# Kernel tuning notes

Measured on AMD Instinct MI355X. Metric: run time of the kernel, lower is better.

The kernel has to match this reference:

```python
import jax, jax.numpy as jnp
import numpy as np

A, B, O, ACT, H, NH = 16, 8192, 128, 16, 128, 4
D = H // NH  # attend_dim
IN = O + ACT
NEG = -1e9


def setup_inputs() -> dict:
    key = jax.random.key(0)
    ks = jax.random.split(key, 16)
    s = lambda k, shape, fan: jax.random.normal(k, shape, jnp.float32) / np.sqrt(fan)
    return {
        "obs": jax.random.normal(ks[0], (A, B, O), jnp.float32),
        "actions": jax.random.uniform(ks[1], (A, B, ACT), jnp.float32),
        # per-agent sa-encoder (enc_fc1)
        "W_sa": s(ks[2], (A, IN, H), IN), "b_sa": jnp.zeros((A, H), jnp.float32),
        # per-agent state encoder (s_enc_fc1)
        "W_s": s(ks[3], (A, O, H), O), "b_s": jnp.zeros((A, H), jnp.float32),
        # shared per-head extractors
        "Wk": s(ks[4], (NH, H, D), H),
        "Wsel": s(ks[5], (NH, H, D), H),
        "Wv": s(ks[6], (NH, H, D), H), "bv": jnp.zeros((NH, D), jnp.float32),
        # per-agent critic MLP
        "Wc1": s(ks[7], (A, 2 * H, H), 2 * H), "bc1": jnp.zeros((A, H), jnp.float32),
        "Wc2": s(ks[8], (A, H, ACT), H), "bc2": jnp.zeros((A, ACT), jnp.float32),
    }


def _bn(x):
    # BatchNorm1d(affine=False) in training mode: normalize over batch axis, biased var
    m = x.mean(axis=1, keepdims=True)
    v = x.var(axis=1, keepdims=True)
    return (x - m) / jnp.sqrt(v + 1e-5)


def reference(obs, actions, W_sa, b_sa, W_s, b_s, Wk, Wsel, Wv, bv, Wc1, bc1, Wc2, bc2):
    lrelu = jax.nn.leaky_relu  # slope 0.01, matches torch default
    inp = jnp.concatenate([obs, actions], axis=-1)            # [A,B,IN]
    sa = lrelu(jnp.einsum('abi,aih->abh', _bn(inp), W_sa) + b_sa[:, None, :])  # [A,B,H]
    se = lrelu(jnp.einsum('abo,aoh->abh', _bn(obs), W_s) + b_s[:, None, :])    # [A,B,H]
    keys = jnp.einsum('abh,nhd->nabd', sa, Wk)                # [NH,A,B,D]
    vals = lrelu(jnp.einsum('abh,nhd->nabd', sa, Wv) + bv[:, None, None, :])
    sel = jnp.einsum('abh,nhd->nabd', se, Wsel)
    logits = jnp.einsum('nibd,njbd->nibj', sel, keys) / np.sqrt(D)  # [NH,A,B,A]
    self_mask = jnp.eye(A, dtype=bool)[None, :, None, :]      # mask j == i
    w = jax.nn.softmax(jnp.where(self_mask, NEG, logits), axis=-1)
    other = jnp.einsum('nibj,njbd->nibd', w, vals)            # [NH,A,B,D]
    other = jnp.transpose(other, (1, 2, 0, 3)).reshape(A, B, NH * D)  # head-order concat
    cin = jnp.concatenate([se, other], axis=-1)               # [A,B,2H]
    h = lrelu(jnp.einsum('abk,akh->abh', cin, Wc1) + bc1[:, None, :])
    all_q = jnp.einsum('abh,aho->abo', h, Wc2) + bc2[:, None, :]      # [A,B,ACT]
    idx = jnp.argmax(actions, axis=-1)[..., None]             # int_acs, [A,B,1]
    q = jnp.take_along_axis(all_q, idx, axis=-1)              # [A,B,1]
    return q
```

## Files before the change

### kernel.cpp

```cpp
#include <hip/hip_runtime.h>
#include <hip/hip_bf16.h>

#define A_N 16
#define B_N 8192
#define O_N 128
#define ACT_N 16
#define H_N 128
#define NH_N 4
#define D_N 32
#define IN_N 144
#define NEGV -1e9f

typedef __attribute__((ext_vector_type(8))) short short8;
typedef __attribute__((ext_vector_type(4))) float floatx4;

static __device__ inline unsigned short f2bf(float f) {
    union { float f; unsigned u; } x{f};
    unsigned u = x.u + 0x7FFFu + ((x.u >> 16) & 1u);
    return (unsigned short)(u >> 16);
}
static __device__ inline unsigned pack_bf2(float a, float b) {
    union { float f; unsigned u; } xa{a}, xb{b};
    unsigned ua = xa.u + 0x7FFFu + ((xa.u >> 16) & 1u);
    unsigned ub = xb.u + 0x7FFFu + ((xb.u >> 16) & 1u);
    return (ua >> 16) | (ub & 0xFFFF0000u);
}
static __device__ inline float bf2f(unsigned short h) {
    union { unsigned u; float f; } x;
    x.u = ((unsigned)h) << 16;
    return x.f;
}
static __device__ inline float bflo(unsigned u) {
    union { unsigned u; float f; } x; x.u = u << 16; return x.f;
}
static __device__ inline float bfhi(unsigned u) {
    union { unsigned u; float f; } x; x.u = u & 0xFFFF0000u; return x.f;
}
static __device__ inline short8 ld_frag(const unsigned* p) {
    union { unsigned u[4]; short8 v; } x;
    uint2 lo = *(const uint2*)p;
    uint2 hi = *(const uint2*)(p + 2);
    x.u[0] = lo.x; x.u[1] = lo.y; x.u[2] = hi.x; x.u[3] = hi.y;
    return x.v;
}

__global__ __launch_bounds__(256) void k_zero(float* p, int n) {
    int i = blockIdx.x * 256 + threadIdx.x;
    if (i < n) p[i] = 0.f;
}

__global__ __launch_bounds__(256) void k_stats(const float* __restrict__ obs,
                                               const float* __restrict__ act,
                                               float* __restrict__ gsum,
                                               float* __restrict__ gsq) {
    __shared__ float ssum[IN_N];
    __shared__ float ssq[IN_N];
    int a = blockIdx.x >> 5;
    int r0 = (blockIdx.x & 31) * 256;
    int t = threadIdx.x;
    if (t < IN_N) { ssum[t] = 0.f; ssq[t] = 0.f; }
    __syncthreads();
    if (t < 128) {
        const float* p = obs + ((size_t)a * B_N + r0) * O_N + t;
        float s = 0.f, q = 0.f;
#pragma unroll 4
        for (int r = 0; r < 256; ++r) {
            float v = p[(size_t)r * O_N];
            s += v; q += v * v;
        }
        ssum[t] = s; ssq[t] = q;
    } else {
        int tt = t - 128;
        int f = tt & 15, rg = tt >> 4;
        const float* p = act + ((size_t)a * B_N + r0 + rg) * ACT_N + f;
        float s = 0.f, q = 0.f;
#pragma unroll 4
        for (int i = 0; i < 32; ++i) {
            float v = p[(size_t)i * 8 * ACT_N];
            s += v; q += v * v;
        }
        atomicAdd(&ssum[O_N + f], s);
        atomicAdd(&ssq[O_N + f], q);
    }
    __syncthreads();
    if (t < IN_N) {
        atomicAdd(&gsum[a * IN_N + t], ssum[t]);
        atomicAdd(&gsq[a * IN_N + t], ssq[t]);
    }
}

__global__ __launch_bounds__(256) void k_finalize(float* gsum, float* gsq) {
    int i = blockIdx.x * 256 + threadIdx.x;
    if (i < A_N * IN_N) {
        const float invB = 1.f / (float)B_N;
        float m = gsum[i] * invB;
        float v = fmaxf(gsq[i] * invB - m * m, 0.f);
        gsum[i] = m;
        gsq[i] = rsqrtf(v + 1e-5f);
    }
}

#define L1E 393216
#define P1E 409600
#define P2E 417792
#define CRE 679936
#define C2E 712704
__global__ __launch_bounds__(256) void k_wprep(
    const float* __restrict__ W_sa, const float* __restrict__ W_s,
    const float* __restrict__ Wk, const float* __restrict__ Wsel,
    const float* __restrict__ Wv, const float* __restrict__ Wc1,
    const float* __restrict__ Wc2, const float* __restrict__ rstd,
    unsigned* __restrict__ wt_l1, unsigned* __restrict__ wt_p1,
    unsigned* __restrict__ wt_p2, unsigned* __restrict__ wt_cr,
    float* __restrict__ wt_c2) {
    int idx = blockIdx.x * 256 + threadIdx.x;
    if (idx < L1E) {
        int a = idx / 24576, rem = idx % 24576;
        int n = rem & 255, kp = rem >> 8;
        int k0 = 2 * kp, k1 = k0 + 1;
        float v0 = 0.f, v1 = 0.f;
        if (n < 128) {
            if (k0 < IN_N) v0 = W_sa[((size_t)a * IN_N + k0) * H_N + n] * rstd[a * IN_N + k0];
            if (k1 < IN_N) v1 = W_sa[((size_t)a * IN_N + k1) * H_N + n] * rstd[a * IN_N + k1];
        } else {
            int m = n - 128;
            if (k0 < O_N) v0 = W_s[((size_t)a * O_N + k0) * H_N + m] * rstd[a * IN_N + k0];
            if (k1 < O_N) v1 = W_s[((size_t)a * O_N + k1) * H_N + m] * rstd[a * IN_N + k1];
        }
        wt_l1[(size_t)a * 24576 + n * 96 + kp] = pack_bf2(v0, v1);
    } else if (idx < P1E) {
        int i2 = idx - L1E;
        int n = i2 & 255, kp = i2 >> 8;
        int k0 = 2 * kp;
        float v0, v1;
        if (n < 128) {
            const float* w = Wk + ((size_t)(n >> 5) * H_N) * D_N + (n & 31);
            v0 = w[(size_t)k0 * D_N]; v1 = w[(size_t)(k0 + 1) * D_N];
        } else {
            int m = n - 128;
            const float* w = Wv + ((size_t)(m >> 5) * H_N) * D_N + (m & 31);
            v0 = w[(size_t)k0 * D_N]; v1 = w[(size_t)(k0 + 1) * D_N];
        }
        wt_p1[n * 64 + kp] = pack_bf2(v0, v1);
    } else if (idx < P2E) {
        int i3 = idx - P1E;
        int n = i3 & 127, kp = i3 >> 7;
        int k0 = 2 * kp;
        const float* w = Wsel + ((size_t)(n >> 5) * H_N) * D_N + (n & 31);
        wt_p2[n * 64 + kp] = pack_bf2(w[(size_t)k0 * D_N], w[(size_t)(k0 + 1) * D_N]);
    } else if (idx < CRE) {
        int i4 = idx - P2E;
        int a = i4 >> 14, r = i4 & 16383;
        int n = r & 127, kp = r >> 7;
        int k0 = 2 * kp;
        const float* w = Wc1 + (size_t)a * 256 * H_N + n;
        wt_cr[(size_t)a * 16384 + n * 128 + kp] =
            pack_bf2(w[(size_t)k0 * H_N], w[(size_t)(k0 + 1) * H_N]);
    } else if (idx < C2E) {
        int i5 = idx - CRE;
        int a = i5 >> 11, rem = i5 & 2047;
        int oo = rem >> 7, h = rem & 127;
        wt_c2[i5] = Wc2[((size_t)a * H_N + h) * ACT_N + oo];
    }
}

__global__ __launch_bounds__(256) void k_bfold(
    const float* __restrict__ mean, const float* __restrict__ rstd,
    const float* __restrict__ W_sa, const float* __restrict__ W_s,
    const float* __restrict__ b_sa, const float* __restrict__ b_s,
    float* __restrict__ fb) {
    int a = blockIdx.x, c = threadIdx.x;
    float s = 0.f;
    if (c < 128) {
        for (int k = 0; k < IN_N; ++k)
            s += mean[a * IN_N + k] * rstd[a * IN_N + k] *
                 W_sa[((size_t)a * IN_N + k) * H_N + c];
        fb[a * 128 + c] = b_sa[a * H_N + c] - s;
    } else {
        int m = c - 128;
        for (int k = 0; k < O_N; ++k)
            s += mean[a * IN_N + k] * rstd[a * IN_N + k] *
                 W_s[((size_t)a * O_N + k) * H_N + m];
        fb[2048 + a * 128 + m] = b_s[a * H_N + m] - s;
    }
}

__global__ __launch_bounds__(512, 2) void k_l1(
    const float* __restrict__ obs, const float* __restrict__ act,
    const unsigned* __restrict__ wt_l1, const float* __restrict__ fb,
    unsigned short* __restrict__ sa_us, unsigned short* __restrict__ se_us,
    int b0g, int Bc) {
    __shared__ unsigned smem[(128 + 256) * 34];
    unsigned* Xs = smem;
    unsigned* Ws = smem + 128 * 34;

    int a = blockIdx.y;
    int b0 = blockIdx.x * 128;
    int t = threadIdx.x;
    int wid = t >> 6, lane = t & 63, lm = lane & 15, lq = lane >> 4;
    int wrow = (wid & 1) * 64;
    int wcol = (wid >> 1) * 64;

    floatx4 acc[4][4];
#pragma unroll
    for (int mt = 0; mt < 4; ++mt)
#pragma unroll
        for (int nt = 0; nt < 4; ++nt)
#pragma unroll
            for (int e = 0; e < 4; ++e) acc[mt][nt][e] = 0.f;

    const unsigned* WtA = wt_l1 + (size_t)a * 24576;

    for (int c = 0; c < 3; ++c) {
        int kk = c * 64;
        __syncthreads();
        for (int idx = t; idx < 128 * 16; idx += 512) {
            int r = idx >> 4, c4 = idx & 15;
            int k = kk + c4 * 4;
            size_t grow = (size_t)a * B_N + b0g + b0 + r;
            float4 v;
            if (k < O_N) v = *(const float4*)&obs[grow * O_N + k];
            else if (k < IN_N) v = *(const float4*)&act[grow * ACT_N + (k - O_N)];
            else v = make_float4(0.f, 0.f, 0.f, 0.f);
            uint2* dst = (uint2*)&Xs[r * 34 + c4 * 2];
            *dst = make_uint2(pack_bf2(v.x, v.y), pack_bf2(v.z, v.w));
        }
        for (int idx = t; idx < 256 * 8; idx += 512) {
            int n = idx >> 3, c4 = idx & 7;
            uint4 w = *(const uint4*)&WtA[(size_t)n * 96 + (kk >> 1) + c4 * 4];
            uint2* dst = (uint2*)&Ws[n * 34 + c4 * 4];
            dst[0] = make_uint2(w.x, w.y);
            dst[1] = make_uint2(w.z, w.w);
        }
        __syncthreads();
#pragma unroll
        for (int s = 0; s < 2; ++s) {
            if (kk + s * 32 >= 160) break;
            short8 afr[4];
#pragma unroll
            for (int mt = 0; mt < 4; ++mt)
                afr[mt] = ld_frag(&Xs[(wrow + mt * 16 + lm) * 34 + s * 16 + lq * 4]);
#pragma unroll
            for (int nt = 0; nt < 4; ++nt) {
                short8 bfr = ld_frag(&Ws[(wcol + nt * 16 + lm) * 34 + s * 16 + lq * 4]);
#pragma unroll
                for (int mt = 0; mt < 4; ++mt)
                    acc[mt][nt] = __builtin_amdgcn_mfma_f32_16x16x32_bf16(
                        afr[mt], bfr, acc[mt][nt], 0, 0, 0);
            }
        }
    }

    int zsel = (wcol >= 128);
    unsigned short* outp = zsel ? se_us : sa_us;
    const float* bias = fb + zsel * 2048 + a * 128;
    int cbase = wcol & 127;
#pragma unroll
    for (int mt = 0; mt < 4; ++mt)
#pragma unroll
        for (int nt = 0; nt < 4; ++nt)
#pragma unroll
            for (int r = 0; r < 4; ++r) {
                int row = wrow + mt * 16 + lq * 4 + r;
                int col = cbase + nt * 16 + lm;
                float v = acc[mt][nt][r] + bias[col];
                v = v > 0.f ? v : 0.01f * v;
                outp[((size_t)(b0 + row) * 16 + a) * 128 + col] = f2bf(v);
            }
}

__global__ __launch_bounds__(256, 3) void k_fused(
    const unsigned* __restrict__ sa_u, const unsigned* __restrict__ se_u,
    const unsigned* __restrict__ wt_p1, const unsigned* __restrict__ wt_p2,
    const float* __restrict__ bv, unsigned short* __restrict__ other_us,
    int Bc) {
    __shared__ unsigned Xs[64 * 66];
    __shared__ unsigned short keys_s[64 * 130];
    __shared__ unsigned short vals_s[64 * 136];
    unsigned short* sel_s = (unsigned short*)Xs;

    int bg0 = blockIdx.x * 4;
    int t = threadIdx.x;
    int wid = t >> 6, lane = t & 63, lm = lane & 15, lq = lane >> 4;
    int wcol = wid * 32;

    const unsigned* sa_base = sa_u + (size_t)(bg0 * 16) * 64;
    const unsigned* se_base = se_u + (size_t)(bg0 * 16) * 64;

    for (int idx = t; idx < 64 * 16; idx += 256) {
        int r = idx >> 4, c4 = idx & 15;
        uint4 v = *(const uint4*)&sa_base[(size_t)idx * 4];
        uint2* dst = (uint2*)&Xs[r * 66 + c4 * 4];
        dst[0] = make_uint2(v.x, v.y);
        dst[1] = make_uint2(v.z, v.w);
    }
    uint4 seR[4];
#pragma unroll
    for (int ii = 0; ii < 4; ++ii) {
        int idx = t + ii * 256;
        seR[ii] = *(const uint4*)&se_base[(size_t)idx * 4];
    }
    __syncthreads();

#pragma unroll
    for (int pass = 0; pass < 2; ++pass) {
        floatx4 acc[4][2];
#pragma unroll
        for (int mt = 0; mt < 4; ++mt)
#pragma unroll
            for (int nt = 0; nt < 2; ++nt)
#pragma unroll
                for (int e = 0; e < 4; ++e) acc[mt][nt][e] = 0.f;
        const unsigned* wbase = wt_p1 + (size_t)(pass * 128) * 64;
#pragma unroll
        for (int s = 0; s < 4; ++s) {
            short8 afr[4];
#pragma unroll
            for (int mt = 0; mt < 4; ++mt)
                afr[mt] = ld_frag(&Xs[(mt * 16 + lm) * 66 + s * 16 + lq * 4]);
#pragma unroll
            for (int nt = 0; nt < 2; ++nt) {
                int col = wcol + nt * 16 + lm;
                short8 bfr = ld_frag(wbase + (size_t)col * 64 + s * 16 + lq * 4);
#pragma unroll
                for (int mt = 0; mt < 4; ++mt)
                    acc[mt][nt] = __builtin_amdgcn_mfma_f32_16x16x32_bf16(
                        afr[mt], bfr, acc[mt][nt], 0, 0, 0);
            }
        }
#pragma unroll
        for (int mt = 0; mt < 4; ++mt)
#pragma unroll
            for (int nt = 0; nt < 2; ++nt)
#pragma unroll
                for (int r = 0; r < 4; ++r) {
                    int row = mt * 16 + lq * 4 + r;
                    int col = wcol + nt * 16 + lm;
                    float v = acc[mt][nt][r];
                    if (pass == 0) {
                        keys_s[row * 130 + col] = f2bf(v);
                    } else {
                        v += bv[col];
                        v = v > 0.f ? v : 0.01f * v;
                        vals_s[row * 136 + col] = f2bf(v);
                    }
                }
    }
    __syncthreads();

#pragma unroll
    for (int ii = 0; ii < 4; ++ii) {
        int idx = t + ii * 256;
        int r = idx >> 4, c4 = idx & 15;
        uint2* dst = (uint2*)&Xs[r * 66 + c4 * 4];
        dst[0] = make_uint2(seR[ii].x, seR[ii].y);
        dst[1] = make_uint2(seR[ii].z, seR[ii].w);
    }
    __syncthreads();

    {
        floatx4 acc[4][2];
#pragma unroll
        for (int mt = 0; mt < 4; ++mt)
#pragma unroll
            for (int nt = 0; nt < 2; ++nt)
#pragma unroll
                for (int e = 0; e < 4; ++e) acc[mt][nt][e] = 0.f;
#pragma unroll
        for (int s = 0; s < 4; ++s) {
            short8 afr[4];
#pragma unroll
            for (int mt = 0; mt < 4; ++mt)
                afr[mt] = ld_frag(&Xs[(mt * 16 + lm) * 66 + s * 16 + lq * 4]);
#pragma unroll
            for (int nt = 0; nt < 2; ++nt) {
                int col = wcol + nt * 16 + lm;
                short8 bfr = ld_frag(wt_p2 + (size_t)col * 64 + s * 16 + lq * 4);
#pragma unroll
                for (int mt = 0; mt < 4; ++mt)
                    acc[mt][nt] = __builtin_amdgcn_mfma_f32_16x16x32_bf16(
                        afr[mt], bfr, acc[mt][nt], 0, 0, 0);
            }
        }
        __syncthreads();
#pragma unroll
        for (int mt = 0; mt < 4; ++mt)
#pragma unroll
            for (int nt = 0; nt < 2; ++nt)
#pragma unroll
                for (int r = 0; r < 4; ++r) {
                    int row = mt * 16 + lq * 4 + r;
                    int col = wcol + nt * 16 + lm;
                    sel_s[row * 132 + col] = f2bf(acc[mt][nt][r]);
                }
    }
    __syncthreads();

    const unsigned* keysU = (const unsigned*)keys_s;
    floatx4 lgacc[4];
#pragma unroll
    for (int n = 0; n < 4; ++n) {
        short8 afr = ld_frag(&Xs[(wid * 16 + lm) * 66 + n * 16 + lq * 4]);
        short8 bfr = ld_frag(&keysU[(wid * 16 + lm) * 65 + n * 16 + lq * 4]);
        floatx4 z4 = {0.f, 0.f, 0.f, 0.f};
        lgacc[n] = __builtin_amdgcn_mfma_f32_16x16x32_bf16(afr, bfr, z4, 0, 0, 0);
    }
    __syncthreads();

    float* lgs = (float*)keys_s;
#pragma unroll
    for (int n = 0; n < 4; ++n)
#pragma unroll
        for (int r = 0; r < 4; ++r) {
            int i = lq * 4 + r;
            lgs[((wid * 4 + n) * 16 + i) * 16 + lm] =
                lgacc[n][r] * 0.17677669529663687f;
        }

    int bsub = wid, n = (t >> 4) & 3, i = t & 15;
    float lg[16];
    {
        const float4* lgp = (const float4*)&lgs[((bsub * 4 + n) * 16 + i) * 16];
#pragma unroll
        for (int c = 0; c < 4; ++c) {
            float4 v = lgp[c];
            lg[4 * c] = v.x; lg[4 * c + 1] = v.y;
            lg[4 * c + 2] = v.z; lg[4 * c + 3] = v.w;
        }
    }
    lg[i] = NEGV;
    float m = lg[0];
#pragma unroll
    for (int j = 1; j < 16; ++j) m = fmaxf(m, lg[j]);
    float sum = 0.f;
#pragma unroll
    for (int j = 0; j < 16; ++j) { lg[j] = __expf(lg[j] - m); sum += lg[j]; }
    float inv = 1.f / sum;
#pragma unroll
    for (int j = 0; j < 16; ++j) lg[j] *= inv;

    const unsigned* valsU = (const unsigned*)vals_s;
    float ov[32];
#pragma unroll
    for (int u = 0; u < 32; ++u) ov[u] = 0.f;
#pragma unroll
    for (int j = 0; j < 16; ++j) {
        const uint4* vrow = (const uint4*)&valsU[(bsub * 16 + j) * 68 + n * 16];
        float w = lg[j];
#pragma unroll
        for (int c = 0; c < 4; ++c) {
            uint4 x = vrow[c];
            ov[8 * c + 0] = fmaf(w, bflo(x.x), ov[8 * c + 0]);
            ov[8 * c + 1] = fmaf(w, bfhi(x.x), ov[8 * c + 1]);
            ov[8 * c + 2] = fmaf(w, bflo(x.y), ov[8 * c + 2]);
            ov[8 * c + 3] = fmaf(w, bfhi(x.y), ov[8 * c + 3]);
            ov[8 * c + 4] = fmaf(w, bflo(x.z), ov[8 * c + 4]);
            ov[8 * c + 5] = fmaf(w, bfhi(x.z), ov[8 * c + 5]);
            ov[8 * c + 6] = fmaf(w, bflo(x.w), ov[8 * c + 6]);
            ov[8 * c + 7] = fmaf(w, bfhi(x.w), ov[8 * c + 7]);
        }
    }
    {
        uint4* orow = (uint4*)&other_us[((size_t)(bg0 + bsub) * 16 + i) * 128 + n * 32];
#pragma unroll
        for (int h = 0; h < 2; ++h) {
            uint4 o;
            o.x = pack_bf2(ov[16 * h + 0], ov[16 * h + 1]);
            o.y = pack_bf2(ov[16 * h + 2], ov[16 * h + 3]);
            o.z = pack_bf2(ov[16 * h + 4], ov[16 * h + 5]);
            o.w = pack_bf2(ov[16 * h + 6], ov[16 * h + 7]);
            orow[2 * h] = o;
            o.x = pack_bf2(ov[16 * h + 8], ov[16 * h + 9]);
            o.y = pack_bf2(ov[16 * h + 10], ov[16 * h + 11]);
            o.z = pack_bf2(ov[16 * h + 12], ov[16 * h + 13]);
            o.w = pack_bf2(ov[16 * h + 14], ov[16 * h + 15]);
            orow[2 * h + 1] = o;
        }
    }
}

__global__ __launch_bounds__(256, 4) void k_critic(
    const unsigned* __restrict__ se_u, const unsigned* __restrict__ other_u,
    const unsigned* __restrict__ wt_cr,
    const float* __restrict__ bc1, const float* __restrict__ actions,
    const float* __restrict__ wt_c2, const float* __restrict__ bc2,
    float* __restrict__ qout, int b0g, int Bc) {
    __shared__ unsigned smem[(64 + 128) * 34];
    unsigned* Xs = smem;
    unsigned* Ws = smem + 64 * 34;

    int a = blockIdx.y;
    int b0 = blockIdx.x * 64;
    int t = threadIdx.x;
    int wid = t >> 6, lane = t & 63, lm = lane & 15, lq = lane >> 4;
    int wrow = (wid & 1) * 32;
    int wcol = (wid >> 1) * 64;

    floatx4 acc[2][4];
#pragma unroll
    for (int mt = 0; mt < 2; ++mt)
#pragma unroll
        for (int nt = 0; nt < 4; ++nt)
#pragma unroll
            for (int e = 0; e < 4; ++e) acc[mt][nt][e] = 0.f;

    const unsigned* WtA = wt_cr + (size_t)a * 16384;

    for (int c = 0; c < 4; ++c) {
        int kk = c * 64;
        __syncthreads();
        const unsigned* src = (c < 2) ? se_u : other_u;
        int off = (c & 1) * 32;
        for (int idx = t; idx < 64 * 8; idx += 256) {
            int r = idx >> 3, c4 = idx & 7;
            uint4 v = *(const uint4*)&src[((size_t)(b0 + r) * 16 + a) * 64 + off + c4 * 4];
            uint2* dst = (uint2*)&Xs[r * 34 + c4 * 4];
            dst[0] = make_uint2(v.x, v.y);
            dst[1] = make_uint2(v.z, v.w);
        }
        for (int idx = t; idx < 128 * 8; idx += 256) {
            int n = idx >> 3, c4 = idx & 7;
            uint4 w = *(const uint4*)&WtA[(size_t)n * 128 + (kk >> 1) + c4 * 4];
            uint2* dst = (uint2*)&Ws[n * 34 + c4 * 4];
            dst[0] = make_uint2(w.x, w.y);
            dst[1] = make_uint2(w.z, w.w);
        }
        __syncthreads();
#pragma unroll
        for (int s = 0; s < 2; ++s) {
            short8 afr[2];
#pragma unroll
            for (int mt = 0; mt < 2; ++mt)
                afr[mt] = ld_frag(&Xs[(wrow + mt * 16 + lm) * 34 + s * 16 + lq * 4]);
#pragma unroll
            for (int nt = 0; nt < 4; ++nt) {
                short8 bfr = ld_frag(&Ws[(wcol + nt * 16 + lm) * 34 + s * 16 + lq * 4]);
#pragma unroll
                for (int mt = 0; mt < 2; ++mt)
                    acc[mt][nt] = __builtin_amdgcn_mfma_f32_16x16x32_bf16(
                        afr[mt], bfr, acc[mt][nt], 0, 0, 0);
            }
        }
    }

    __syncthreads();
    unsigned short* hbuf = (unsigned short*)smem;
#pragma unroll
    for (int mt = 0; mt < 2; ++mt)
#pragma unroll
        for (int nt = 0; nt < 4; ++nt)
#pragma unroll
            for (int r = 0; r < 4; ++r) {
                int row = wrow + mt * 16 + lq * 4 + r;
                int col = wcol + nt * 16 + lm;
                float v = acc[mt][nt][r] + bc1[a * H_N + col];
                v = v > 0.f ? v : 0.01f * v;
                hbuf[row * 132 + col] = f2bf(v);
            }
    __syncthreads();
    if (t < 64) {
        size_t arow = (size_t)a * B_N + b0g + b0 + t;
        const float* ap = &actions[arow * ACT_N];
        float bestv = ap[0];
        int bi = 0;
        for (int o = 1; o < ACT_N; ++o) {
            float v = ap[o];
            if (v > bestv) { bestv = v; bi = o; }
        }
        float q = bc2[a * ACT_N + bi];
        const float4* w4p = (const float4*)&wt_c2[((size_t)a * ACT_N + bi) * H_N];
        const uint2* hp2 = (const uint2*)&hbuf[t * 132];
#pragma unroll
        for (int h4 = 0; h4 < 32; ++h4) {
            float4 w4 = w4p[h4];
            uint2 hh = hp2[h4];
            q = fmaf(bflo(hh.x), w4.x, q);
            q = fmaf(bfhi(hh.x), w4.y, q);
            q = fmaf(bflo(hh.y), w4.z, q);
            q = fmaf(bfhi(hh.y), w4.w, q);
        }
        qout[arow] = q;
    }
}

extern "C" void kernel_launch(void* const* d_in, const int* in_sizes, int n_in,
                              void* d_out, int out_size, void* d_ws, size_t ws_size,
                              hipStream_t stream) {
    const float* obs     = (const float*)d_in[0];
    const float* actions = (const float*)d_in[1];
    const float* W_sa    = (const float*)d_in[2];
    const float* b_sa    = (const float*)d_in[3];
    const float* W_s     = (const float*)d_in[4];
    const float* b_s     = (const float*)d_in[5];
    const float* Wk      = (const float*)d_in[6];
    const float* Wsel    = (const float*)d_in[7];
    const float* Wv      = (const float*)d_in[8];
    const float* bv      = (const float*)d_in[9];
    const float* Wc1     = (const float*)d_in[10];
    const float* bc1     = (const float*)d_in[11];
    const float* Wc2     = (const float*)d_in[12];
    const float* bc2     = (const float*)d_in[13];
    float* out = (float*)d_out;
    char* ws = (char*)d_ws;

    size_t o = 0;
    float* gsum = (float*)(ws + o); o += 2304 * 4;
    float* gsq  = (float*)(ws + o); o += 2304 * 4;
    unsigned* wt_l1 = (unsigned*)(ws + o); o += (size_t)393216 * 4;
    unsigned* wt_p1 = (unsigned*)(ws + o); o += (size_t)16384 * 4;
    unsigned* wt_p2 = (unsigned*)(ws + o); o += (size_t)8192 * 4;
    unsigned* wt_cr = (unsigned*)(ws + o); o += (size_t)262144 * 4;
    float* fb = (float*)(ws + o); o += (size_t)4096 * 4;
    float* wt_c2 = (float*)(ws + o); o += (size_t)32768 * 4;
    size_t fixed = o;

    int Bc = B_N;
    while (Bc > 128 && fixed + 12288ull * Bc > ws_size) Bc >>= 1;

    unsigned short* sa_us = (unsigned short*)(ws + o); o += (size_t)A_N * Bc * 128 * 2;
    unsigned short* se_us = (unsigned short*)(ws + o); o += (size_t)A_N * Bc * 128 * 2;
    unsigned short* ot_us = (unsigned short*)(ws + o); o += (size_t)A_N * Bc * 128 * 2;

    k_zero<<<dim3(18), 256, 0, stream>>>(gsum, 2 * A_N * IN_N);
    k_stats<<<dim3(A_N * 32), 256, 0, stream>>>(obs, actions, gsum, gsq);
    k_finalize<<<dim3(9), 256, 0, stream>>>(gsum, gsq);
    k_wprep<<<dim3(C2E / 256), 256, 0, stream>>>(W_sa, W_s, Wk, Wsel, Wv, Wc1, Wc2,
                                                 gsq, wt_l1, wt_p1, wt_p2, wt_cr, wt_c2);
    k_bfold<<<dim3(A_N), 256, 0, stream>>>(gsum, gsq, W_sa, W_s, b_sa, b_s, fb);

    for (int b0g = 0; b0g < B_N; b0g += Bc) {
        k_l1<<<dim3(Bc / 128, A_N), 512, 0, stream>>>(
            obs, actions, wt_l1, fb, sa_us, se_us, b0g, Bc);
        k_fused<<<dim3(Bc / 4), 256, 0, stream>>>(
            (const unsigned*)sa_us, (const unsigned*)se_us, wt_p1, wt_p2, bv,
            ot_us, Bc);
        k_critic<<<dim3(Bc / 64, A_N), 256, 0, stream>>>(
            (const unsigned*)se_us, (const unsigned*)ot_us, wt_cr, bc1,
            actions, wt_c2, bc2, out, b0g, Bc);
    }
}
```

Measured before the change: 317.7 us.

## Make fused attention kernel wave-private, dropping block-wide barriers and shared input staging

```diff
diff --git a/kernel.cpp b/kernel.cpp
--- a/kernel.cpp
+++ b/kernel.cpp
@@ -41,6 +41,11 @@
     uint2 lo = *(const uint2*)p;
     uint2 hi = *(const uint2*)(p + 2);
     x.u[0] = lo.x; x.u[1] = lo.y; x.u[2] = hi.x; x.u[3] = hi.y;
+    return x.v;
+}
+static __device__ inline short8 ld_frag4(const unsigned* p) {
+    union { uint4 q; short8 v; } x;
+    x.q = *(const uint4*)p;
     return x.v;
 }
 
@@ -274,153 +279,98 @@
     const unsigned* __restrict__ wt_p1, const unsigned* __restrict__ wt_p2,
     const float* __restrict__ bv, unsigned short* __restrict__ other_us,
     int Bc) {
-    __shared__ unsigned Xs[64 * 66];
-    __shared__ unsigned short keys_s[64 * 130];
-    __shared__ unsigned short vals_s[64 * 136];
-    unsigned short* sel_s = (unsigned short*)Xs;
-
-    int bg0 = blockIdx.x * 4;
+    __shared__ unsigned short lds[4][3][16][136];
+
     int t = threadIdx.x;
     int wid = t >> 6, lane = t & 63, lm = lane & 15, lq = lane >> 4;
-    int wcol = wid * 32;
-
-    const unsigned* sa_base = sa_u + (size_t)(bg0 * 16) * 64;
-    const unsigned* se_base = se_u + (size_t)(bg0 * 16) * 64;
-
-    for (int idx = t; idx < 64 * 16; idx += 256) {
-        int r = idx >> 4, c4 = idx & 15;
-        uint4 v = *(const uint4*)&sa_base[(size_t)idx * 4];
-        uint2* dst = (uint2*)&Xs[r * 66 + c4 * 4];
-        dst[0] = make_uint2(v.x, v.y);
-        dst[1] = make_uint2(v.z, v.w);
-    }
-    uint4 seR[4];
-#pragma unroll
-    for (int ii = 0; ii < 4; ++ii) {
-        int idx = t + ii * 256;
-        seR[ii] = *(const uint4*)&se_base[(size_t)idx * 4];
-    }
-    __syncthreads();
-
-#pragma unroll
-    for (int pass = 0; pass < 2; ++pass) {
-        floatx4 acc[4][2];
-#pragma unroll
-        for (int mt = 0; mt < 4; ++mt)
-#pragma unroll
-            for (int nt = 0; nt < 2; ++nt)
-#pragma unroll
-                for (int e = 0; e < 4; ++e) acc[mt][nt][e] = 0.f;
-        const unsigned* wbase = wt_p1 + (size_t)(pass * 128) * 64;
-#pragma unroll
-        for (int s = 0; s < 4; ++s) {
-            short8 afr[4];
-#pragma unroll
-            for (int mt = 0; mt < 4; ++mt)
-                afr[mt] = ld_frag(&Xs[(mt * 16 + lm) * 66 + s * 16 + lq * 4]);
-#pragma unroll
-            for (int nt = 0; nt < 2; ++nt) {
-                int col = wcol + nt * 16 + lm;
-                short8 bfr = ld_frag(wbase + (size_t)col * 64 + s * 16 + lq * 4);
-#pragma unroll
-                for (int mt = 0; mt < 4; ++mt)
-                    acc[mt][nt] = __builtin_amdgcn_mfma_f32_16x16x32_bf16(
-                        afr[mt], bfr, acc[mt][nt], 0, 0, 0);
-            }
-        }
-#pragma unroll
-        for (int mt = 0; mt < 4; ++mt)
-#pragma unroll
-            for (int nt = 0; nt < 2; ++nt)
-#pragma unroll
-                for (int r = 0; r < 4; ++r) {
-                    int row = mt * 16 + lq * 4 + r;
-                    int col = wcol + nt * 16 + lm;
-                    float v = acc[mt][nt][r];
-                    if (pass == 0) {
-                        keys_s[row * 130 + col] = f2bf(v);
-                    } else {
-                        v += bv[col];
-                        v = v > 0.f ? v : 0.01f * v;
-                        vals_s[row * 136 + col] = f2bf(v);
-                    }
-                }
-    }
-    __syncthreads();
-
-#pragma unroll
-    for (int ii = 0; ii < 4; ++ii) {
-        int idx = t + ii * 256;
-        int r = idx >> 4, c4 = idx & 15;
-        uint2* dst = (uint2*)&Xs[r * 66 + c4 * 4];
-        dst[0] = make_uint2(seR[ii].x, seR[ii].y);
-        dst[1] = make_uint2(seR[ii].z, seR[ii].w);
-    }
-    __syncthreads();
-
-    {
-        floatx4 acc[4][2];
-#pragma unroll
-        for (int mt = 0; mt < 4; ++mt)
-#pragma unroll
-            for (int nt = 0; nt < 2; ++nt)
-#pragma unroll
-                for (int e = 0; e < 4; ++e) acc[mt][nt][e] = 0.f;
-#pragma unroll
-        for (int s = 0; s < 4; ++s) {
-            short8 afr[4];
-#pragma unroll
-            for (int mt = 0; mt < 4; ++mt)
-                afr[mt] = ld_frag(&Xs[(mt * 16 + lm) * 66 + s * 16 + lq * 4]);
-#pragma unroll
-            for (int nt = 0; nt < 2; ++nt) {
-                int col = wcol + nt * 16 + lm;
-                short8 bfr = ld_frag(wt_p2 + (size_t)col * 64 + s * 16 + lq * 4);
-#pragma unroll
-                for (int mt = 0; mt < 4; ++mt)
-                    acc[mt][nt] = __builtin_amdgcn_mfma_f32_16x16x32_bf16(
-                        afr[mt], bfr, acc[mt][nt], 0, 0, 0);
-            }
-        }
-        __syncthreads();
-#pragma unroll
-        for (int mt = 0; mt < 4; ++mt)
-#pragma unroll
-            for (int nt = 0; nt < 2; ++nt)
-#pragma unroll
-                for (int r = 0; r < 4; ++r) {
-                    int row = mt * 16 + lq * 4 + r;
-                    int col = wcol + nt * 16 + lm;
-                    sel_s[row * 132 + col] = f2bf(acc[mt][nt][r]);
-                }
-    }
-    __syncthreads();
-
-    const unsigned* keysU = (const unsigned*)keys_s;
+    int b = blockIdx.x * 4 + wid;
+
+    unsigned short* keysS = &lds[wid][0][0][0];
+    unsigned short* valsS = &lds[wid][1][0][0];
+    unsigned short* selS  = &lds[wid][2][0][0];
+
+    const unsigned* sap = sa_u + (size_t)b * 1024;
+    const unsigned* sep = se_u + (size_t)b * 1024;
+
+    short8 saf[4], sef[4];
+#pragma unroll
+    for (int s = 0; s < 4; ++s) saf[s] = ld_frag4(sap + lm * 64 + s * 16 + lq * 4);
+#pragma unroll
+    for (int s = 0; s < 4; ++s) sef[s] = ld_frag4(sep + lm * 64 + s * 16 + lq * 4);
+
+#pragma unroll
+    for (int ct = 0; ct < 8; ++ct) {
+        floatx4 acc = {0.f, 0.f, 0.f, 0.f};
+        const unsigned* wb = wt_p1 + (size_t)(ct * 16 + lm) * 64 + lq * 4;
+#pragma unroll
+        for (int s = 0; s < 4; ++s)
+            acc = __builtin_amdgcn_mfma_f32_16x16x32_bf16(saf[s], ld_frag4(wb + s * 16),
+                                                          acc, 0, 0, 0);
+        int col = ct * 16 + lm;
+#pragma unroll
+        for (int r = 0; r < 4; ++r)
+            keysS[(lq * 4 + r) * 136 + col] = f2bf(acc[r]);
+    }
+#pragma unroll
+    for (int ct = 0; ct < 8; ++ct) {
+        floatx4 acc = {0.f, 0.f, 0.f, 0.f};
+        const unsigned* wb = wt_p1 + (size_t)(128 + ct * 16 + lm) * 64 + lq * 4;
+#pragma unroll
+        for (int s = 0; s < 4; ++s)
+            acc = __builtin_amdgcn_mfma_f32_16x16x32_bf16(saf[s], ld_frag4(wb + s * 16),
+                                                          acc, 0, 0, 0);
+        int col = ct * 16 + lm;
+        float bvc = bv[col];
+#pragma unroll
+        for (int r = 0; r < 4; ++r) {
+            float v = acc[r] + bvc;
+            v = v > 0.f ? v : 0.01f * v;
+            valsS[(lq * 4 + r) * 136 + col] = f2bf(v);
+        }
+    }
+#pragma unroll
+    for (int ct = 0; ct < 8; ++ct) {
+        floatx4 acc = {0.f, 0.f, 0.f, 0.f};
+        const unsigned* wb = wt_p2 + (size_t)(ct * 16 + lm) * 64 + lq * 4;
+#pragma unroll
+        for (int s = 0; s < 4; ++s)
+            acc = __builtin_amdgcn_mfma_f32_16x16x32_bf16(sef[s], ld_frag4(wb + s * 16),
+                                                          acc, 0, 0, 0);
+        int col = ct * 16 + lm;
+#pragma unroll
+        for (int r = 0; r < 4; ++r)
+            selS[(lq * 4 + r) * 136 + col] = f2bf(acc[r]);
+    }
+
+    asm volatile("" ::: "memory");
+
+    const unsigned* selU = (const unsigned*)selS;
+    const unsigned* keysU = (const unsigned*)keysS;
     floatx4 lgacc[4];
 #pragma unroll
     for (int n = 0; n < 4; ++n) {
-        short8 afr = ld_frag(&Xs[(wid * 16 + lm) * 66 + n * 16 + lq * 4]);
-        short8 bfr = ld_frag(&keysU[(wid * 16 + lm) * 65 + n * 16 + lq * 4]);
+        short8 af = ld_frag(selU + lm * 68 + n * 16 + lq * 4);
+        short8 bf = ld_frag(keysU + lm * 68 + n * 16 + lq * 4);
         floatx4 z4 = {0.f, 0.f, 0.f, 0.f};
-        lgacc[n] = __builtin_amdgcn_mfma_f32_16x16x32_bf16(afr, bfr, z4, 0, 0, 0);
-    }
-    __syncthreads();
-
-    float* lgs = (float*)keys_s;
+        lgacc[n] = __builtin_amdgcn_mfma_f32_16x16x32_bf16(af, bf, z4, 0, 0, 0);
+    }
+
+    asm volatile("" ::: "memory");
+
+    float* lgs = (float*)selS;
 #pragma unroll
     for (int n = 0; n < 4; ++n)
 #pragma unroll
-        for (int r = 0; r < 4; ++r) {
-            int i = lq * 4 + r;
-            lgs[((wid * 4 + n) * 16 + i) * 16 + lm] =
+        for (int r = 0; r < 4; ++r)
+            lgs[(n * 16 + lq * 4 + r) * 16 + lm] =
                 lgacc[n][r] * 0.17677669529663687f;
-        }
-
-    int bsub = wid, n = (t >> 4) & 3, i = t & 15;
+
+    asm volatile("" ::: "memory");
+
+    int n2 = lq, i2 = lm;
     float lg[16];
     {
-        const float4* lgp = (const float4*)&lgs[((bsub * 4 + n) * 16 + i) * 16];
+        const float4* lgp = (const float4*)&lgs[(n2 * 16 + i2) * 16];
 #pragma unroll
         for (int c = 0; c < 4; ++c) {
             float4 v = lgp[c];
@@ -428,7 +378,7 @@
             lg[4 * c + 2] = v.z; lg[4 * c + 3] = v.w;
         }
     }
-    lg[i] = NEGV;
+    lg[i2] = NEGV;
     float m = lg[0];
 #pragma unroll
     for (int j = 1; j < 16; ++j) m = fmaxf(m, lg[j]);
@@ -439,13 +389,13 @@
 #pragma unroll
     for (int j = 0; j < 16; ++j) lg[j] *= inv;
 
-    const unsigned* valsU = (const unsigned*)vals_s;
+    const unsigned* valsU = (const unsigned*)valsS;
     float ov[32];
 #pragma unroll
     for (int u = 0; u < 32; ++u) ov[u] = 0.f;
 #pragma unroll
     for (int j = 0; j < 16; ++j) {
-        const uint4* vrow = (const uint4*)&valsU[(bsub * 16 + j) * 68 + n * 16];
+        const uint4* vrow = (const uint4*)(valsU + j * 68 + n2 * 16);
         float w = lg[j];
 #pragma unroll
         for (int c = 0; c < 4; ++c) {
@@ -461,7 +411,7 @@
         }
     }
     {
-        uint4* orow = (uint4*)&other_us[((size_t)(bg0 + bsub) * 16 + i) * 128 + n * 32];
+        uint4* orow = (uint4*)&other_us[((size_t)b * 16 + i2) * 128 + n2 * 32];
 #pragma unroll
         for (int h = 0; h < 2; ++h) {
             uint4 o;
```

After: 336.9 us. +6.0%, slower.

## Prefetch next K-chunk into registers during MFMA in layer-1 and critic GEMMs

Applied to the files above, without the earlier changes.

```diff
diff --git a/kernel.cpp b/kernel.cpp
--- a/kernel.cpp
+++ b/kernel.cpp
@@ -41,6 +41,11 @@
     uint2 lo = *(const uint2*)p;
     uint2 hi = *(const uint2*)(p + 2);
     x.u[0] = lo.x; x.u[1] = lo.y; x.u[2] = hi.x; x.u[3] = hi.y;
+    return x.v;
+}
+static __device__ inline short8 ld_frag4(const unsigned* p) {
+    union { uint4 q; short8 v; } x;
+    x.q = *(const uint4*)p;
     return x.v;
 }
 
@@ -211,31 +216,50 @@
 
     const unsigned* WtA = wt_l1 + (size_t)a * 24576;
 
-    for (int c = 0; c < 3; ++c) {
-        int kk = c * 64;
-        __syncthreads();
-        for (int idx = t; idx < 128 * 16; idx += 512) {
+    float4 xr[4];
+    auto loadx = [&](int cc) {
+#pragma unroll
+        for (int i = 0; i < 4; ++i) {
+            int idx = t + i * 512;
             int r = idx >> 4, c4 = idx & 15;
-            int k = kk + c4 * 4;
+            int k = cc * 64 + c4 * 4;
             size_t grow = (size_t)a * B_N + b0g + b0 + r;
-            float4 v;
-            if (k < O_N) v = *(const float4*)&obs[grow * O_N + k];
-            else if (k < IN_N) v = *(const float4*)&act[grow * ACT_N + (k - O_N)];
-            else v = make_float4(0.f, 0.f, 0.f, 0.f);
+            if (k < O_N) xr[i] = *(const float4*)&obs[grow * O_N + k];
+            else if (k < IN_N) xr[i] = *(const float4*)&act[grow * ACT_N + (k - O_N)];
+            else xr[i] = make_float4(0.f, 0.f, 0.f, 0.f);
+        }
+    };
+    auto writex = [&]() {
+#pragma unroll
+        for (int i = 0; i < 4; ++i) {
+            int idx = t + i * 512;
+            int r = idx >> 4, c4 = idx & 15;
             uint2* dst = (uint2*)&Xs[r * 34 + c4 * 2];
-            *dst = make_uint2(pack_bf2(v.x, v.y), pack_bf2(v.z, v.w));
-        }
-        for (int idx = t; idx < 256 * 8; idx += 512) {
+            *dst = make_uint2(pack_bf2(xr[i].x, xr[i].y), pack_bf2(xr[i].z, xr[i].w));
+        }
+    };
+    auto stagew = [&](int cc) {
+#pragma unroll
+        for (int i = 0; i < 4; ++i) {
+            int idx = t + i * 512;
             int n = idx >> 3, c4 = idx & 7;
-            uint4 w = *(const uint4*)&WtA[(size_t)n * 96 + (kk >> 1) + c4 * 4];
+            uint4 w = *(const uint4*)&WtA[(size_t)n * 96 + cc * 32 + c4 * 4];
             uint2* dst = (uint2*)&Ws[n * 34 + c4 * 4];
             dst[0] = make_uint2(w.x, w.y);
             dst[1] = make_uint2(w.z, w.w);
         }
-        __syncthreads();
+    };
+
+    loadx(0);
+    writex();
+    stagew(0);
+    __syncthreads();
+
+    for (int c = 0; c < 3; ++c) {
+        if (c < 2) loadx(c + 1);
 #pragma unroll
         for (int s = 0; s < 2; ++s) {
-            if (kk + s * 32 >= 160) break;
+            if (c * 64 + s * 32 >= 160) break;
             short8 afr[4];
 #pragma unroll
             for (int mt = 0; mt < 4; ++mt)
@@ -248,6 +272,12 @@
                     acc[mt][nt] = __builtin_amdgcn_mfma_f32_16x16x32_bf16(
                         afr[mt], bfr, acc[mt][nt], 0, 0, 0);
             }
+        }
+        __syncthreads();
+        if (c < 2) {
+            writex();
+            stagew(c + 1);
+            __syncthreads();
         }
     }
 
@@ -282,7 +312,6 @@
     int bg0 = blockIdx.x * 4;
     int t = threadIdx.x;
     int wid = t >> 6, lane = t & 63, lm = lane & 15, lq = lane >> 4;
-    int wcol = wid * 32;
 
     const unsigned* sa_base = sa_u + (size_t)(bg0 * 16) * 64;
     const unsigned* se_base = se_u + (size_t)(bg0 * 16) * 64;
@@ -296,22 +325,18 @@
     }
     uint4 seR[4];
 #pragma unroll
-    for (int ii = 0; ii < 4; ++ii) {
-        int idx = t + ii * 256;
-        seR[ii] = *(const uint4*)&se_base[(size_t)idx * 4];
-    }
-    __syncthreads();
-
-#pragma unroll
-    for (int pass = 0; pass < 2; ++pass) {
-        floatx4 acc[4][2];
+    for (int ii = 0; ii < 4; ++ii)
+        seR[ii] = *(const uint4*)&se_base[(size_t)(t + ii * 256) * 4];
+    __syncthreads();
+
+    {
+        floatx4 acc[4][4];
 #pragma unroll
         for (int mt = 0; mt < 4; ++mt)
 #pragma unroll
-            for (int nt = 0; nt < 2; ++nt)
+            for (int nt = 0; nt < 4; ++nt)
 #pragma unroll
                 for (int e = 0; e < 4; ++e) acc[mt][nt][e] = 0.f;
-        const unsigned* wbase = wt_p1 + (size_t)(pass * 128) * 64;
 #pragma unroll
         for (int s = 0; s < 4; ++s) {
             short8 afr[4];
@@ -319,32 +344,42 @@
             for (int mt = 0; mt < 4; ++mt)
                 afr[mt] = ld_frag(&Xs[(mt * 16 + lm) * 66 + s * 16 + lq * 4]);
 #pragma unroll
-            for (int nt = 0; nt < 2; ++nt) {
-                int col = wcol + nt * 16 + lm;
-                short8 bfr = ld_frag(wbase + (size_t)col * 64 + s * 16 + lq * 4);
+            for (int nt = 0; nt < 4; ++nt) {
+                int col = wid * 64 + nt * 16 + lm;
+                short8 bfr = ld_frag4(wt_p1 + (size_t)col * 64 + s * 16 + lq * 4);
 #pragma unroll
                 for (int mt = 0; mt < 4; ++mt)
                     acc[mt][nt] = __builtin_amdgcn_mfma_f32_16x16x32_bf16(
                         afr[mt], bfr, acc[mt][nt], 0, 0, 0);
             }
         }
-#pragma unroll
-        for (int mt = 0; mt < 4; ++mt)
-#pragma unroll
-            for (int nt = 0; nt < 2; ++nt)
-#pragma unroll
-                for (int r = 0; r < 4; ++r) {
-                    int row = mt * 16 + lq * 4 + r;
-                    int col = wcol + nt * 16 + lm;
-                    float v = acc[mt][nt][r];
-                    if (pass == 0) {
-                        keys_s[row * 130 + col] = f2bf(v);
-                    } else {
-                        v += bv[col];
+        if (wid < 2) {
+#pragma unroll
+            for (int mt = 0; mt < 4; ++mt)
+#pragma unroll
+                for (int nt = 0; nt < 4; ++nt)
+#pragma unroll
+                    for (int r = 0; r < 4; ++r) {
+                        int row = mt * 16 + lq * 4 + r;
+                        int col = wid * 64 + nt * 16 + lm;
+                        keys_s[row * 130 + col] = f2bf(acc[mt][nt][r]);
+                    }
+        } else {
+#pragma unroll
+            for (int mt = 0; mt < 4; ++mt)
+#pragma unroll
+                for (int nt = 0; nt < 4; ++nt) {
+                    int col = (wid - 2) * 64 + nt * 16 + lm;
+                    float bvc = bv[col];
+#pragma unroll
+                    for (int r = 0; r < 4; ++r) {
+                        int row = mt * 16 + lq * 4 + r;
+                        float v = acc[mt][nt][r] + bvc;
                         v = v > 0.f ? v : 0.01f * v;
                         vals_s[row * 136 + col] = f2bf(v);
                     }
                 }
+        }
     }
     __syncthreads();
 
@@ -359,6 +394,7 @@
     __syncthreads();
 
     {
+        int wcol = wid * 32;
         floatx4 acc[4][2];
 #pragma unroll
         for (int mt = 0; mt < 4; ++mt)
@@ -375,7 +411,7 @@
 #pragma unroll
             for (int nt = 0; nt < 2; ++nt) {
                 int col = wcol + nt * 16 + lm;
-                short8 bfr = ld_frag(wt_p2 + (size_t)col * 64 + s * 16 + lq * 4);
+                short8 bfr = ld_frag4(wt_p2 + (size_t)col * 64 + s * 16 + lq * 4);
 #pragma unroll
                 for (int mt = 0; mt < 4; ++mt)
                     acc[mt][nt] = __builtin_amdgcn_mfma_f32_16x16x32_bf16(
@@ -400,10 +436,10 @@
     floatx4 lgacc[4];
 #pragma unroll
     for (int n = 0; n < 4; ++n) {
-        short8 afr = ld_frag(&Xs[(wid * 16 + lm) * 66 + n * 16 + lq * 4]);
-        short8 bfr = ld_frag(&keysU[(wid * 16 + lm) * 65 + n * 16 + lq * 4]);
+        short8 af = ld_frag(&Xs[(wid * 16 + lm) * 66 + n * 16 + lq * 4]);
+        short8 bf = ld_frag(&keysU[(wid * 16 + lm) * 65 + n * 16 + lq * 4]);
         floatx4 z4 = {0.f, 0.f, 0.f, 0.f};
-        lgacc[n] = __builtin_amdgcn_mfma_f32_16x16x32_bf16(afr, bfr, z4, 0, 0, 0);
+        lgacc[n] = __builtin_amdgcn_mfma_f32_16x16x32_bf16(af, bf, z4, 0, 0, 0);
     }
     __syncthreads();
 
@@ -506,26 +542,48 @@
 
     const unsigned* WtA = wt_cr + (size_t)a * 16384;
 
+    uint4 xr[2], wr[4];
+    auto loadxw = [&](int cc) {
+        const unsigned* src = (cc < 2) ? se_u : other_u;
+        int off = (cc & 1) * 32;
+#pragma unroll
+        for (int i = 0; i < 2; ++i) {
+            int idx = t + i * 256;
+            int r = idx >> 3, c4 = idx & 7;
+            xr[i] = *(const uint4*)&src[((size_t)(b0 + r) * 16 + a) * 64 + off + c4 * 4];
+        }
+#pragma unroll
+        for (int i = 0; i < 4; ++i) {
+            int idx = t + i * 256;
+            int n = idx >> 3, c4 = idx & 7;
+            wr[i] = *(const uint4*)&WtA[(size_t)n * 128 + cc * 32 + c4 * 4];
+        }
+    };
+    auto writexw = [&]() {
+#pragma unroll
+        for (int i = 0; i < 2; ++i) {
+            int idx = t + i * 256;
+            int r = idx >> 3, c4 = idx & 7;
+            uint2* dst = (uint2*)&Xs[r * 34 + c4 * 4];
+            dst[0] = make_uint2(xr[i].x, xr[i].y);
+            dst[1] = make_uint2(xr[i].z, xr[i].w);
+        }
+#pragma unroll
+        for (int i = 0; i < 4; ++i) {
+            int idx = t + i * 256;
+            int n = idx >> 3, c4 = idx & 7;
+            uint2* dst = (uint2*)&Ws[n * 34 + c4 * 4];
+            dst[0] = make_uint2(wr[i].x, wr[i].y);
+            dst[1] = make_uint2(wr[i].z, wr[i].w);
+        }
+    };
+
+    loadxw(0);
+    writexw();
+    __syncthreads();
+
     for (int c = 0; c < 4; ++c) {
-        int kk = c * 64;
-        __syncthreads();
-        const unsigned* src = (c < 2) ? se_u : other_u;
-        int off = (c & 1) * 32;
-        for (int idx = t; idx < 64 * 8; idx += 256) {
-            int r = idx >> 3, c4 = idx & 7;
-            uint4 v = *(const uint4*)&src[((size_t)(b0 + r) * 16 + a) * 64 + off + c4 * 4];
-            uint2* dst = (uint2*)&Xs[r * 34 + c4 * 4];
-            dst[0] = make_uint2(v.x, v.y);
-            dst[1] = make_uint2(v.z, v.w);
-        }
-        for (int idx = t; idx < 128 * 8; idx += 256) {
-            int n = idx >> 3, c4 = idx & 7;
-            uint4 w = *(const uint4*)&WtA[(size_t)n * 128 + (kk >> 1) + c4 * 4];
-            uint2* dst = (uint2*)&Ws[n * 34 + c4 * 4];
-            dst[0] = make_uint2(w.x, w.y);
-            dst[1] = make_uint2(w.z, w.w);
-        }
-        __syncthreads();
+        if (c < 3) loadxw(c + 1);
 #pragma unroll
         for (int s = 0; s < 2; ++s) {
             short8 afr[2];
@@ -541,9 +599,13 @@
                         afr[mt], bfr, acc[mt][nt], 0, 0, 0);
             }
         }
-    }
-
-    __syncthreads();
+        __syncthreads();
+        if (c < 3) {
+            writexw();
+            __syncthreads();
+        }
+    }
+
     unsigned short* hbuf = (unsigned short*)smem;
 #pragma unroll
     for (int mt = 0; mt < 2; ++mt)
```

New measurement: 306.1 us. -3.6%, faster.

## Load fused-kernel MFMA fragments from global and vectorize BN stats reads

Applied to the files above, without the earlier changes.

```diff
diff --git a/kernel.cpp b/kernel.cpp
--- a/kernel.cpp
+++ b/kernel.cpp
@@ -43,6 +43,11 @@
     x.u[0] = lo.x; x.u[1] = lo.y; x.u[2] = hi.x; x.u[3] = hi.y;
     return x.v;
 }
+static __device__ inline short8 ld_frag4(const unsigned* p) {
+    union { uint4 q; short8 v; } x;
+    x.q = *(const uint4*)p;
+    return x.v;
+}
 
 __global__ __launch_bounds__(256) void k_zero(float* p, int n) {
     int i = blockIdx.x * 256 + threadIdx.x;
@@ -55,27 +60,35 @@
                                                float* __restrict__ gsq) {
     __shared__ float ssum[IN_N];
     __shared__ float ssq[IN_N];
-    int a = blockIdx.x >> 5;
-    int r0 = (blockIdx.x & 31) * 256;
+    int a = blockIdx.x >> 4;
+    int r0 = (blockIdx.x & 15) * 512;
     int t = threadIdx.x;
     if (t < IN_N) { ssum[t] = 0.f; ssq[t] = 0.f; }
     __syncthreads();
+    {
+        int c0 = (t & 31) * 4, rg = t >> 5;
+        const float* p = obs + ((size_t)a * B_N + r0 + rg) * O_N + c0;
+        float s0 = 0.f, s1 = 0.f, s2 = 0.f, s3 = 0.f;
+        float q0 = 0.f, q1 = 0.f, q2 = 0.f, q3 = 0.f;
+#pragma unroll 4
+        for (int i = 0; i < 64; ++i) {
+            float4 v = *(const float4*)(p + (size_t)i * 8 * O_N);
+            s0 += v.x; q0 += v.x * v.x;
+            s1 += v.y; q1 += v.y * v.y;
+            s2 += v.z; q2 += v.z * v.z;
+            s3 += v.w; q3 += v.w * v.w;
+        }
+        atomicAdd(&ssum[c0 + 0], s0); atomicAdd(&ssq[c0 + 0], q0);
+        atomicAdd(&ssum[c0 + 1], s1); atomicAdd(&ssq[c0 + 1], q1);
+        atomicAdd(&ssum[c0 + 2], s2); atomicAdd(&ssq[c0 + 2], q2);
+        atomicAdd(&ssum[c0 + 3], s3); atomicAdd(&ssq[c0 + 3], q3);
+    }
     if (t < 128) {
-        const float* p = obs + ((size_t)a * B_N + r0) * O_N + t;
-        float s = 0.f, q = 0.f;
-#pragma unroll 4
-        for (int r = 0; r < 256; ++r) {
-            float v = p[(size_t)r * O_N];
-            s += v; q += v * v;
-        }
-        ssum[t] = s; ssq[t] = q;
-    } else {
-        int tt = t - 128;
-        int f = tt & 15, rg = tt >> 4;
+        int f = t & 15, rg = t >> 4;
         const float* p = act + ((size_t)a * B_N + r0 + rg) * ACT_N + f;
         float s = 0.f, q = 0.f;
 #pragma unroll 4
-        for (int i = 0; i < 32; ++i) {
+        for (int i = 0; i < 64; ++i) {
             float v = p[(size_t)i * 8 * ACT_N];
             s += v; q += v * v;
         }
@@ -274,91 +287,73 @@
     const unsigned* __restrict__ wt_p1, const unsigned* __restrict__ wt_p2,
     const float* __restrict__ bv, unsigned short* __restrict__ other_us,
     int Bc) {
-    __shared__ unsigned Xs[64 * 66];
     __shared__ unsigned short keys_s[64 * 130];
     __shared__ unsigned short vals_s[64 * 136];
-    unsigned short* sel_s = (unsigned short*)Xs;
+    __shared__ unsigned short sel_s[64 * 132];
 
     int bg0 = blockIdx.x * 4;
     int t = threadIdx.x;
     int wid = t >> 6, lane = t & 63, lm = lane & 15, lq = lane >> 4;
-    int wcol = wid * 32;
 
     const unsigned* sa_base = sa_u + (size_t)(bg0 * 16) * 64;
     const unsigned* se_base = se_u + (size_t)(bg0 * 16) * 64;
 
-    for (int idx = t; idx < 64 * 16; idx += 256) {
-        int r = idx >> 4, c4 = idx & 15;
-        uint4 v = *(const uint4*)&sa_base[(size_t)idx * 4];
-        uint2* dst = (uint2*)&Xs[r * 66 + c4 * 4];
-        dst[0] = make_uint2(v.x, v.y);
-        dst[1] = make_uint2(v.z, v.w);
-    }
-    uint4 seR[4];
-#pragma unroll
-    for (int ii = 0; ii < 4; ++ii) {
-        int idx = t + ii * 256;
-        seR[ii] = *(const uint4*)&se_base[(size_t)idx * 4];
-    }
-    __syncthreads();
-
-#pragma unroll
-    for (int pass = 0; pass < 2; ++pass) {
-        floatx4 acc[4][2];
+    {
+        floatx4 acc[4][4];
 #pragma unroll
         for (int mt = 0; mt < 4; ++mt)
 #pragma unroll
-            for (int nt = 0; nt < 2; ++nt)
+            for (int nt = 0; nt < 4; ++nt)
 #pragma unroll
                 for (int e = 0; e < 4; ++e) acc[mt][nt][e] = 0.f;
-        const unsigned* wbase = wt_p1 + (size_t)(pass * 128) * 64;
 #pragma unroll
         for (int s = 0; s < 4; ++s) {
             short8 afr[4];
 #pragma unroll
             for (int mt = 0; mt < 4; ++mt)
-                afr[mt] = ld_frag(&Xs[(mt * 16 + lm) * 66 + s * 16 + lq * 4]);
-#pragma unroll
-            for (int nt = 0; nt < 2; ++nt) {
-                int col = wcol + nt * 16 + lm;
-                short8 bfr = ld_frag(wbase + (size_t)col * 64 + s * 16 + lq * 4);
+                afr[mt] = ld_frag4(sa_base + (size_t)(mt * 16 + lm) * 64 + s * 16 + lq * 4);
+#pragma unroll
+            for (int nt = 0; nt < 4; ++nt) {
+                int col = wid * 64 + nt * 16 + lm;
+                short8 bfr = ld_frag4(wt_p1 + (size_t)col * 64 + s * 16 + lq * 4);
 #pragma unroll
                 for (int mt = 0; mt < 4; ++mt)
                     acc[mt][nt] = __builtin_amdgcn_mfma_f32_16x16x32_bf16(
                         afr[mt], bfr, acc[mt][nt], 0, 0, 0);
             }
         }
-#pragma unroll
-        for (int mt = 0; mt < 4; ++mt)
-#pragma unroll
-            for (int nt = 0; nt < 2; ++nt)
-#pragma unroll
-                for (int r = 0; r < 4; ++r) {
-                    int row = mt * 16 + lq * 4 + r;
-                    int col = wcol + nt * 16 + lm;
-                    float v = acc[mt][nt][r];
-                    if (pass == 0) {
-                        keys_s[row * 130 + col] = f2bf(v);
-                    } else {
-                        v += bv[col];
+        if (wid < 2) {
+#pragma unroll
+            for (int mt = 0; mt < 4; ++mt)
+#pragma unroll
+                for (int nt = 0; nt < 4; ++nt)
+#pragma unroll
+                    for (int r = 0; r < 4; ++r) {
+                        int row = mt * 16 + lq * 4 + r;
+                        int col = wid * 64 + nt * 16 + lm;
+                        keys_s[row * 130 + col] = f2bf(acc[mt][nt][r]);
+                    }
+        } else {
+#pragma unroll
+            for (int mt = 0; mt < 4; ++mt)
+#pragma unroll
+                for (int nt = 0; nt < 4; ++nt) {
+                    int col = (wid - 2) * 64 + nt * 16 + lm;
+                    float bvc = bv[col];
+#pragma unroll
+                    for (int r = 0; r < 4; ++r) {
+                        int row = mt * 16 + lq * 4 + r;
+                        float v = acc[mt][nt][r] + bvc;
                         v = v > 0.f ? v : 0.01f * v;
                         vals_s[row * 136 + col] = f2bf(v);
                     }
                 }
+        }
     }
     __syncthreads();
 
-#pragma unroll
-    for (int ii = 0; ii < 4; ++ii) {
-        int idx = t + ii * 256;
-        int r = idx >> 4, c4 = idx & 15;
-        uint2* dst = (uint2*)&Xs[r * 66 + c4 * 4];
-        dst[0] = make_uint2(seR[ii].x, seR[ii].y);
-        dst[1] = make_uint2(seR[ii].z, seR[ii].w);
-    }
-    __syncthreads();
-
     {
+        int wcol = wid * 32;
         floatx4 acc[4][2];
 #pragma unroll
         for (int mt = 0; mt < 4; ++mt)
@@ -371,18 +366,17 @@
             short8 afr[4];
 #pragma unroll
             for (int mt = 0; mt < 4; ++mt)
-                afr[mt] = ld_frag(&Xs[(mt * 16 + lm) * 66 + s * 16 + lq * 4]);
+                afr[mt] = ld_frag4(se_base + (size_t)(mt * 16 + lm) * 64 + s * 16 + lq * 4);
 #pragma unroll
             for (int nt = 0; nt < 2; ++nt) {
                 int col = wcol + nt * 16 + lm;
-                short8 bfr = ld_frag(wt_p2 + (size_t)col * 64 + s * 16 + lq * 4);
+                short8 bfr = ld_frag4(wt_p2 + (size_t)col * 64 + s * 16 + lq * 4);
 #pragma unroll
                 for (int mt = 0; mt < 4; ++mt)
                     acc[mt][nt] = __builtin_amdgcn_mfma_f32_16x16x32_bf16(
                         afr[mt], bfr, acc[mt][nt], 0, 0, 0);
             }
         }
-        __syncthreads();
 #pragma unroll
         for (int mt = 0; mt < 4; ++mt)
 #pragma unroll
@@ -396,14 +390,15 @@
     }
     __syncthreads();
 
+    const unsigned* selU = (const unsigned*)sel_s;
     const unsigned* keysU = (const unsigned*)keys_s;
     floatx4 lgacc[4];
 #pragma unroll
     for (int n = 0; n < 4; ++n) {
-        short8 afr = ld_frag(&Xs[(wid * 16 + lm) * 66 + n * 16 + lq * 4]);
-        short8 bfr = ld_frag(&keysU[(wid * 16 + lm) * 65 + n * 16 + lq * 4]);
+        short8 af = ld_frag(&selU[(wid * 16 + lm) * 66 + n * 16 + lq * 4]);
+        short8 bf = ld_frag(&keysU[(wid * 16 + lm) * 65 + n * 16 + lq * 4]);
         floatx4 z4 = {0.f, 0.f, 0.f, 0.f};
-        lgacc[n] = __builtin_amdgcn_mfma_f32_16x16x32_bf16(afr, bfr, z4, 0, 0, 0);
+        lgacc[n] = __builtin_amdgcn_mfma_f32_16x16x32_bf16(af, bf, z4, 0, 0, 0);
     }
     __syncthreads();
 
@@ -416,6 +411,7 @@
             lgs[((wid * 4 + n) * 16 + i) * 16 + lm] =
                 lgacc[n][r] * 0.17677669529663687f;
         }
+    asm volatile("" ::: "memory");
 
     int bsub = wid, n = (t >> 4) & 3, i = t & 15;
     float lg[16];
@@ -622,7 +618,7 @@
     unsigned short* ot_us = (unsigned short*)(ws + o); o += (size_t)A_N * Bc * 128 * 2;
 
     k_zero<<<dim3(18), 256, 0, stream>>>(gsum, 2 * A_N * IN_N);
-    k_stats<<<dim3(A_N * 32), 256, 0, stream>>>(obs, actions, gsum, gsq);
+    k_stats<<<dim3(A_N * 16), 256, 0, stream>>>(obs, actions, gsum, gsq);
     k_finalize<<<dim3(9), 256, 0, stream>>>(gsum, gsq);
     k_wprep<<<dim3(C2E / 256), 256, 0, stream>>>(W_sa, W_s, Wk, Wsel, Wv, Wc1, Wc2,
                                                  gsq, wt_l1, wt_p1, wt_p2, wt_cr, wt_c2);
```

After: 299.4 us. 5.7% less time.
